# Performance work log

Measured on AMD Instinct MI355X. Metric: run time of the kernel, lower is better.

Reference implementation:

```python
import jax, jax.numpy as jnp
import numpy as np

NUM_LEAVES = 256
EPS = 1e-6
SHARPNESS = 1.0   # init_sharpness, non-trainable buffer
BIAS_SHIFT = -2.0


def _generalized_gcd(w1, w2, lambd):
    # lambd: per-node bias -> andness via sigmoid; broadcast over batch
    lam = jax.nn.sigmoid(lambd)
    a = jnp.abs(w1) + EPS
    b = jnp.abs(w2) + EPS
    return lam * jnp.minimum(a, b) + (1.0 - lam) * jnp.maximum(a, b)


def setup_inputs() -> dict:
    key = jax.random.key(0)
    ks = jax.random.split(key, 6)
    B, L = 65536, NUM_LEAVES
    x = jax.random.normal(ks[0], (B, L), jnp.float32)
    # xavier-like scale for the leaf projection
    W_leaf = jax.random.normal(ks[1], (L, L), jnp.float32) * (1.0 / np.sqrt(L))
    weights = jax.random.uniform(ks[2], (L - 1, 2), jnp.float32, 0.5, 1.5)
    biases = jax.random.uniform(ks[3], (L - 1,), jnp.float32) * 0.1
    w_out = jax.random.normal(ks[4], (1, 1), jnp.float32)
    b_out = jnp.full((1,), 0.5, jnp.float32)
    return {"x": x, "W_leaf": W_leaf, "weights": weights,
            "biases": biases, "w_out": w_out, "b_out": b_out}


def reference(x, W_leaf, weights, biases, w_out, b_out):
    # InputToLeafFC: sigmoid(sharpness * (x @ W^T + bias_shift))
    leaf = jax.nn.sigmoid(SHARPNESS * (x @ W_leaf.T + BIAS_SHIFT))  # (B, L)

    # The original pops two nodes from the front of the queue and appends the
    # result; for a power-of-two leaf count this is exactly a level-by-level
    # pairwise tree reduction, with node weights consumed in order.
    cur = leaf
    off = 0
    n = cur.shape[1]
    while n > 1:  # log2(L) levels, each fully vectorized over (batch, pairs)
        m = n // 2
        w = weights[off:off + m]   # (m, 2)
        b = biases[off:off + m]    # (m,)
        left = cur[:, 0::2] * w[:, 0]
        right = cur[:, 1::2] * w[:, 1]
        cur = _generalized_gcd(left, right, b)  # (B, m)
        off += m
        n = m
    # fc_out: Linear(1,1) then sigmoid -> (B, 1)
    return jax.nn.sigmoid(cur * w_out[0, 0] + b_out[0])
```

## Files before the change

### kernel.cpp

```cpp
#include <hip/hip_runtime.h>
#include <stdint.h>


#define EPS 1e-6f
#define LOG2E 1.44269504088896340736f
#define PARAM_OFF 131072

typedef __attribute__((ext_vector_type(8))) short short8;
typedef __attribute__((ext_vector_type(4))) short short4_t;
typedef __attribute__((ext_vector_type(4))) float float4_t;

__device__ __forceinline__ float fast_sigmoid(float z) {
    float e = __builtin_amdgcn_exp2f(-z * LOG2E);
    return __builtin_amdgcn_rcpf(1.0f + e);
}

__device__ __forceinline__ short f2bf(float f) {
    uint32_t u = __builtin_bit_cast(uint32_t, f);
    u += 0x7FFFu + ((u >> 16) & 1u);
    return (short)(u >> 16);
}

__device__ __forceinline__ short8 pack8(float4 a, float4 b) {
    short8 s;
    s[0] = f2bf(a.x); s[1] = f2bf(a.y); s[2] = f2bf(a.z); s[3] = f2bf(a.w);
    s[4] = f2bf(b.x); s[5] = f2bf(b.y); s[6] = f2bf(b.z); s[7] = f2bf(b.w);
    return s;
}

__device__ __forceinline__ float ggcd(float l, float r, float lam) {
    float a = fabsf(l) + EPS;
    float b = fabsf(r) + EPS;
    float mn = fminf(a, b);
    float mx = fmaxf(a, b);
    return fmaf(lam, mn - mx, mx);
}

__device__ __forceinline__ void lds16(const void* g, void* l) {
    __builtin_amdgcn_global_load_lds(
        (const __attribute__((address_space(1))) unsigned int*)g,
        (__attribute__((address_space(3))) unsigned int*)l, 16, 0, 0);
}

__device__ __forceinline__ void tree_reduce(float4_t acc[16], int c0,
                                            const float4* pv, float res[4]) {
    #pragma unroll
    for (int t = 0; t < 16; ++t) {
        #pragma unroll
        for (int r = 0; r < 4; ++r) acc[t][r] = fast_sigmoid(acc[t][r] - 2.0f);
    }
    #pragma unroll
    for (int tp = 0; tp < 8; ++tp) {
        float4 p = pv[c0 * 8 + tp];
        #pragma unroll
        for (int r = 0; r < 4; ++r)
            acc[tp][r] = ggcd(acc[2*tp][r] * p.x, acc[2*tp+1][r] * p.y, p.z);
    }
    #pragma unroll
    for (int tp = 0; tp < 4; ++tp) {
        float4 p = pv[128 + c0 * 4 + tp];
        #pragma unroll
        for (int r = 0; r < 4; ++r)
            acc[tp][r] = ggcd(acc[2*tp][r] * p.x, acc[2*tp+1][r] * p.y, p.z);
    }
    #pragma unroll
    for (int tp = 0; tp < 2; ++tp) {
        float4 p = pv[192 + c0 * 2 + tp];
        #pragma unroll
        for (int r = 0; r < 4; ++r)
            acc[tp][r] = ggcd(acc[2*tp][r] * p.x, acc[2*tp+1][r] * p.y, p.z);
    }
    {
        float4 p = pv[224 + c0];
        #pragma unroll
        for (int r = 0; r < 4; ++r)
            res[r] = ggcd(acc[0][r] * p.x, acc[1][r] * p.y, p.z);
    }
}

__global__ __launch_bounds__(256)
void convert_w(const float* __restrict__ Wl, const float* __restrict__ wts,
               const float* __restrict__ bia, char* __restrict__ img) {
    int i = blockIdx.x * 256 + threadIdx.x;
    int a = i * 8;
    int t    = a >> 14;
    int s    = a & 16383;
    int j    = s >> 6;
    int b    = s & 63;
    int cpos = b >> 4;
    int h    = (b >> 3) & 1;
    int c    = cpos ^ (j & 3);
    int k    = t * 32 + c * 8 + h * 4;
    int src  = ((j & 15) << 4) | (j >> 4);
    float4 w4 = *(const float4*)&Wl[src * 256 + k];
    short4_t s4;
    s4.x = f2bf(w4.x); s4.y = f2bf(w4.y); s4.z = f2bf(w4.z); s4.w = f2bf(w4.w);
    *(short4_t*)&img[a] = s4;

    if (i < 255) {
        float4* pv = (float4*)(img + PARAM_OFF);
        pv[i] = make_float4(wts[2 * i], wts[2 * i + 1], fast_sigmoid(bia[i]), 0.f);
    } else if (i == 255) {
        ((float4*)(img + PARAM_OFF))[255] = make_float4(0.f, 0.f, 0.f, 0.f);
    }
}

__global__ __launch_bounds__(256, 4)
void btln_main(const float* __restrict__ x, const char* __restrict__ img,
               const float* __restrict__ wout, const float* __restrict__ bout,
               float* __restrict__ out) {
    __shared__ short Wt[2][8192];
    __shared__ float4 pv[256];

    const int tid  = threadIdx.x;
    const int lane = tid & 63;
    const int wv   = tid >> 6;
    const int c0   = lane & 15;
    const int q    = lane >> 4;

    pv[tid] = ((const float4*)(img + PARAM_OFF))[tid];

    #pragma unroll
    for (int p = 0; p < 4; ++p)
        lds16(img + p * 4096 + tid * 16, (char*)Wt[0] + p * 4096 + tid * 16);

    const int rowbase = blockIdx.x * 64 + wv * 16;
    const float* xr = x + (size_t)(rowbase + c0) * 256;

    float4_t acc[16];
    #pragma unroll
    for (int t = 0; t < 16; ++t) acc[t] = (float4_t){0.f, 0.f, 0.f, 0.f};

    float4 a0 = *(const float4*)(xr + q * 8);
    float4 a1 = *(const float4*)(xr + q * 8 + 4);

    __syncthreads();

    const int vx = c0 & 3;
    #pragma unroll 1
    for (int kt = 0; kt < 8; ++kt) {
        const short* cur = Wt[kt & 1];
        if (kt < 7) {
            const char* g = img + (kt + 1) * 16384 + tid * 16;
            char* l = (char*)Wt[(kt + 1) & 1] + tid * 16;
            #pragma unroll
            for (int p = 0; p < 4; ++p)
                lds16(g + p * 4096, l + p * 4096);
        }
        const int kn = (kt < 7 ? kt + 1 : 7) * 32;
        float4 n0 = *(const float4*)(xr + kn + q * 8);
        float4 n1 = *(const float4*)(xr + kn + q * 8 + 4);

        short8 af = pack8(a0, a1);
        #pragma unroll
        for (int t = 0; t < 16; ++t) {
            const short* base = &cur[(t * 16 + c0) * 32];
            short8 bf = *(const short8*)&base[(q ^ vx) * 8];
            acc[t] = __builtin_amdgcn_mfma_f32_16x16x32_bf16(af, bf, acc[t], 0, 0, 0);
        }
        __syncthreads();
        a0 = n0; a1 = n1;
    }

    float res[4];
    tree_reduce(acc, c0, pv, res);

    const int offs[4] = {240, 248, 252, 254};
    #pragma unroll
    for (int k = 0; k < 4; ++k) {
        float4 p = pv[offs[k] + (c0 >> (k + 1))];
        bool isLeft = ((c0 >> k) & 1) == 0;
        #pragma unroll
        for (int r = 0; r < 4; ++r) {
            float other = __shfl_xor(res[r], 1 << k, 64);
            float lf = isLeft ? res[r] : other;
            float rt = isLeft ? other  : res[r];
            res[r] = ggcd(lf * p.x, rt * p.y, p.z);
        }
    }

    if (c0 == 0) {
        const float wo = wout[0];
        const float bo = bout[0];
        #pragma unroll
        for (int r = 0; r < 4; ++r)
            out[rowbase + q * 4 + r] = fast_sigmoid(fmaf(res[r], wo, bo));
    }
}

extern "C" void kernel_launch(void* const* d_in, const int* in_sizes, int n_in,
                              void* d_out, int out_size, void* d_ws, size_t ws_size,
                              hipStream_t stream) {
    const float* x   = (const float*)d_in[0];
    const float* Wl  = (const float*)d_in[1];
    const float* wts = (const float*)d_in[2];
    const float* bia = (const float*)d_in[3];
    const float* wo  = (const float*)d_in[4];
    const float* bo  = (const float*)d_in[5];
    float* out = (float*)d_out;
    char* img = (char*)d_ws;

    convert_w<<<dim3(64), dim3(256), 0, stream>>>(Wl, wts, bia, img);

    const int rows = out_size;
    dim3 grid(rows / 64), block(256);
    btln_main<<<grid, block, 0, stream>>>(x, img, wo, bo, out);
}
```

Measured before the change: 118.0 us.

## Keep full bf16 weight matrix resident in LDS and use 32x32 MFMA tiles

Loads the whole 256x256 bf16 leaf weight matrix into shared memory once per block instead of streaming 32-wide K slices with double buffering, which removes the per-step barrier. Blocks grow to 512 threads covering 256 rows, so each wave handles 32 rows with 32x32x16 MFMAs and the weight load is amortised over more rows. The tree reduction is rewritten for the new accumulator layout, with one extra shuffle level. The cost is 128KB of LDS per block, which caps occupancy, and larger register use from the 16-wide accumulators.

```diff
diff --git a/kernel.cpp b/kernel.cpp
--- a/kernel.cpp
+++ b/kernel.cpp
@@ -6,9 +6,9 @@
 #define LOG2E 1.44269504088896340736f
 #define PARAM_OFF 131072
 
-typedef __attribute__((ext_vector_type(8))) short short8;
-typedef __attribute__((ext_vector_type(4))) short short4_t;
-typedef __attribute__((ext_vector_type(4))) float float4_t;
+typedef __attribute__((ext_vector_type(8)))  short short8;
+typedef __attribute__((ext_vector_type(4)))  short short4_t;
+typedef __attribute__((ext_vector_type(16))) float float16_t;
 
 __device__ __forceinline__ float fast_sigmoid(float z) {
     float e = __builtin_amdgcn_exp2f(-z * LOG2E);
@@ -42,149 +42,128 @@
         (__attribute__((address_space(3))) unsigned int*)l, 16, 0, 0);
 }
 
-__device__ __forceinline__ void tree_reduce(float4_t acc[16], int c0,
-                                            const float4* pv, float res[4]) {
-    #pragma unroll
-    for (int t = 0; t < 16; ++t) {
-        #pragma unroll
-        for (int r = 0; r < 4; ++r) acc[t][r] = fast_sigmoid(acc[t][r] - 2.0f);
-    }
-    #pragma unroll
-    for (int tp = 0; tp < 8; ++tp) {
-        float4 p = pv[c0 * 8 + tp];
-        #pragma unroll
-        for (int r = 0; r < 4; ++r)
-            acc[tp][r] = ggcd(acc[2*tp][r] * p.x, acc[2*tp+1][r] * p.y, p.z);
-    }
-    #pragma unroll
-    for (int tp = 0; tp < 4; ++tp) {
-        float4 p = pv[128 + c0 * 4 + tp];
-        #pragma unroll
-        for (int r = 0; r < 4; ++r)
-            acc[tp][r] = ggcd(acc[2*tp][r] * p.x, acc[2*tp+1][r] * p.y, p.z);
-    }
-    #pragma unroll
-    for (int tp = 0; tp < 2; ++tp) {
-        float4 p = pv[192 + c0 * 2 + tp];
-        #pragma unroll
-        for (int r = 0; r < 4; ++r)
-            acc[tp][r] = ggcd(acc[2*tp][r] * p.x, acc[2*tp+1][r] * p.y, p.z);
-    }
-    {
-        float4 p = pv[224 + c0];
-        #pragma unroll
-        for (int r = 0; r < 4; ++r)
-            res[r] = ggcd(acc[0][r] * p.x, acc[1][r] * p.y, p.z);
-    }
-}
-
 __global__ __launch_bounds__(256)
 void convert_w(const float* __restrict__ Wl, const float* __restrict__ wts,
                const float* __restrict__ bia, char* __restrict__ img) {
     int i = blockIdx.x * 256 + threadIdx.x;
-    int a = i * 8;
-    int t    = a >> 14;
-    int s    = a & 16383;
-    int j    = s >> 6;
-    int b    = s & 63;
-    int cpos = b >> 4;
-    int h    = (b >> 3) & 1;
-    int c    = cpos ^ (j & 3);
-    int k    = t * 32 + c * 8 + h * 4;
-    int src  = ((j & 15) << 4) | (j >> 4);
+    int a   = i * 8;
+    int h   = i & 1;
+    int pos = (i >> 1) & 31;
+    int j   = i >> 6;
+    int c_i = pos ^ (j & 31);
+    int k   = c_i * 8 + h * 4;
+    int src = ((j & 31) << 3) | (j >> 5);
     float4 w4 = *(const float4*)&Wl[src * 256 + k];
     short4_t s4;
     s4.x = f2bf(w4.x); s4.y = f2bf(w4.y); s4.z = f2bf(w4.z); s4.w = f2bf(w4.w);
     *(short4_t*)&img[a] = s4;
 
     if (i < 255) {
-        float4* pv = (float4*)(img + PARAM_OFF);
-        pv[i] = make_float4(wts[2 * i], wts[2 * i + 1], fast_sigmoid(bia[i]), 0.f);
+        float4* pvg = (float4*)(img + PARAM_OFF);
+        pvg[i] = make_float4(wts[2 * i], wts[2 * i + 1], fast_sigmoid(bia[i]), 0.f);
     } else if (i == 255) {
         ((float4*)(img + PARAM_OFF))[255] = make_float4(0.f, 0.f, 0.f, 0.f);
     }
 }
 
-__global__ __launch_bounds__(256, 4)
+__global__ __launch_bounds__(512, 2)
 void btln_main(const float* __restrict__ x, const char* __restrict__ img,
                const float* __restrict__ wout, const float* __restrict__ bout,
                float* __restrict__ out) {
-    __shared__ short Wt[2][8192];
+    __shared__ short Ws[65536];
     __shared__ float4 pv[256];
 
     const int tid  = threadIdx.x;
     const int lane = tid & 63;
     const int wv   = tid >> 6;
-    const int c0   = lane & 15;
-    const int q    = lane >> 4;
+    const int c    = lane & 31;
+    const int hi   = lane >> 5;
 
-    pv[tid] = ((const float4*)(img + PARAM_OFF))[tid];
+    if (tid < 256) pv[tid] = ((const float4*)(img + PARAM_OFF))[tid];
 
     #pragma unroll
-    for (int p = 0; p < 4; ++p)
-        lds16(img + p * 4096 + tid * 16, (char*)Wt[0] + p * 4096 + tid * 16);
+    for (int p = 0; p < 16; ++p)
+        lds16(img + p * 8192 + tid * 16, (char*)Ws + p * 8192 + tid * 16);
 
-    const int rowbase = blockIdx.x * 64 + wv * 16;
-    const float* xr = x + (size_t)(rowbase + c0) * 256;
+    const int rowbase = blockIdx.x * 256 + wv * 32;
+    const float* xr = x + (size_t)(rowbase + c) * 256 + hi * 8;
 
-    float4_t acc[16];
+    float16_t acc[8];
     #pragma unroll
-    for (int t = 0; t < 16; ++t) acc[t] = (float4_t){0.f, 0.f, 0.f, 0.f};
+    for (int t = 0; t < 8; ++t)
+        acc[t] = (float16_t){0.f,0.f,0.f,0.f,0.f,0.f,0.f,0.f,
+                             0.f,0.f,0.f,0.f,0.f,0.f,0.f,0.f};
 
-    float4 a0 = *(const float4*)(xr + q * 8);
-    float4 a1 = *(const float4*)(xr + q * 8 + 4);
+    float4 a0 = *(const float4*)(xr);
+    float4 a1 = *(const float4*)(xr + 4);
 
     __syncthreads();
 
-    const int vx = c0 & 3;
+    const int cbase = c * 512;
     #pragma unroll 1
-    for (int kt = 0; kt < 8; ++kt) {
-        const short* cur = Wt[kt & 1];
-        if (kt < 7) {
-            const char* g = img + (kt + 1) * 16384 + tid * 16;
-            char* l = (char*)Wt[(kt + 1) & 1] + tid * 16;
-            #pragma unroll
-            for (int p = 0; p < 4; ++p)
-                lds16(g + p * 4096, l + p * 4096);
+    for (int s = 0; s < 16; ++s) {
+        float4 n0 = a0, n1 = a1;
+        if (s < 15) {
+            n0 = *(const float4*)(xr + (s + 1) * 16);
+            n1 = *(const float4*)(xr + (s + 1) * 16 + 4);
         }
-        const int kn = (kt < 7 ? kt + 1 : 7) * 32;
-        float4 n0 = *(const float4*)(xr + kn + q * 8);
-        float4 n1 = *(const float4*)(xr + kn + q * 8 + 4);
-
         short8 af = pack8(a0, a1);
+        const int boff = cbase + (((s * 2 + hi) ^ c) << 4);
         #pragma unroll
-        for (int t = 0; t < 16; ++t) {
-            const short* base = &cur[(t * 16 + c0) * 32];
-            short8 bf = *(const short8*)&base[(q ^ vx) * 8];
-            acc[t] = __builtin_amdgcn_mfma_f32_16x16x32_bf16(af, bf, acc[t], 0, 0, 0);
+        for (int t = 0; t < 8; ++t) {
+            short8 bf = *(const short8*)((const char*)Ws + t * 16384 + boff);
+            acc[t] = __builtin_amdgcn_mfma_f32_32x32x16_bf16(af, bf, acc[t], 0, 0, 0);
         }
-        __syncthreads();
         a0 = n0; a1 = n1;
     }
 
-    float res[4];
-    tree_reduce(acc, c0, pv, res);
+    float4 p10 = pv[c * 4 + 0], p11 = pv[c * 4 + 1];
+    float4 p12 = pv[c * 4 + 2], p13 = pv[c * 4 + 3];
+    float4 p20 = pv[128 + c * 2 + 0], p21 = pv[128 + c * 2 + 1];
+    float4 p3  = pv[192 + c];
 
-    const int offs[4] = {240, 248, 252, 254};
+    float res[16];
     #pragma unroll
-    for (int k = 0; k < 4; ++k) {
-        float4 p = pv[offs[k] + (c0 >> (k + 1))];
-        bool isLeft = ((c0 >> k) & 1) == 0;
+    for (int r = 0; r < 16; ++r) {
+        float s0 = fast_sigmoid(acc[0][r] - 2.0f);
+        float s1 = fast_sigmoid(acc[1][r] - 2.0f);
+        float s2 = fast_sigmoid(acc[2][r] - 2.0f);
+        float s3 = fast_sigmoid(acc[3][r] - 2.0f);
+        float s4 = fast_sigmoid(acc[4][r] - 2.0f);
+        float s5 = fast_sigmoid(acc[5][r] - 2.0f);
+        float s6 = fast_sigmoid(acc[6][r] - 2.0f);
+        float s7 = fast_sigmoid(acc[7][r] - 2.0f);
+        float u0 = ggcd(s0 * p10.x, s1 * p10.y, p10.z);
+        float u1 = ggcd(s2 * p11.x, s3 * p11.y, p11.z);
+        float u2 = ggcd(s4 * p12.x, s5 * p12.y, p12.z);
+        float u3 = ggcd(s6 * p13.x, s7 * p13.y, p13.z);
+        float v0 = ggcd(u0 * p20.x, u1 * p20.y, p20.z);
+        float v1 = ggcd(u2 * p21.x, u3 * p21.y, p21.z);
+        res[r]   = ggcd(v0 * p3.x,  v1 * p3.y,  p3.z);
+    }
+
+    const int offs[5] = {224, 240, 248, 252, 254};
+    #pragma unroll
+    for (int k = 0; k < 5; ++k) {
+        float4 p = pv[offs[k] + (c >> (k + 1))];
+        bool isLeft = ((c >> k) & 1) == 0;
         #pragma unroll
-        for (int r = 0; r < 4; ++r) {
-            float other = __shfl_xor(res[r], 1 << k, 64);
-            float lf = isLeft ? res[r] : other;
-            float rt = isLeft ? other  : res[r];
+        for (int r = 0; r < 16; ++r) {
+            float o = __shfl_xor(res[r], 1 << k, 64);
+            float lf = isLeft ? res[r] : o;
+            float rt = isLeft ? o      : res[r];
             res[r] = ggcd(lf * p.x, rt * p.y, p.z);
         }
     }
 
-    if (c0 == 0) {
+    if (c == 0) {
         const float wo = wout[0];
         const float bo = bout[0];
         #pragma unroll
-        for (int r = 0; r < 4; ++r)
-            out[rowbase + q * 4 + r] = fast_sigmoid(fmaf(res[r], wo, bo));
+        for (int r = 0; r < 16; ++r) {
+            int row = (r & 3) + ((r >> 2) << 3) + (hi << 2);
+            out[rowbase + row] = fast_sigmoid(fmaf(res[r], wo, bo));
+        }
     }
 }
 
@@ -203,6 +182,6 @@
     convert_w<<<dim3(64), dim3(256), 0, stream>>>(Wl, wts, bia, img);
 
     const int rows = out_size;
-    dim3 grid(rows / 64), block(256);
+    dim3 grid(rows / 256), block(512);
     btln_main<<<grid, block, 0, stream>>>(x, img, wo, bo, out);
 }
```

After: 118.4 us. Within noise of the previous version (+0.3%).
